# Kernel optimization log

Hardware: AMD Instinct MI355X
Metric: run time of the kernel (lower is better)

## Reference

```python
import jax, jax.numpy as jnp
import numpy as np

N_POINTS = 1_000_000
NUM_PILLARS = 30_000
BN_EPS = 1e-3


def _bn(x, gamma, beta, mean, var):
    # eval-mode BatchNorm1d with eps=0.001
    return (x - mean) * (gamma * jax.lax.rsqrt(var + BN_EPS)) + beta


def setup_inputs() -> dict:
    key = jax.random.key(0)
    ks = jax.random.split(key, 5)
    C1, C2 = 32, 64
    return {
        "points": jax.random.normal(ks[0], (N_POINTS, 5), dtype=jnp.float32),
        "f_center": jax.random.normal(ks[1], (N_POINTS, 3), dtype=jnp.float32),
        "unq_inv": jax.random.randint(ks[2], (N_POINTS,), 0, NUM_PILLARS, dtype=jnp.int32),
        "W1": jax.random.normal(ks[3], (7, C1), dtype=jnp.float32) * 0.1,
        "g1": jnp.ones((C1,), jnp.float32),
        "b1": jnp.zeros((C1,), jnp.float32),
        "m1": jnp.zeros((C1,), jnp.float32),
        "v1": jnp.ones((C1,), jnp.float32),
        "W2": jax.random.normal(ks[4], (C2, C1), dtype=jnp.float32) * 0.1,
        "g2": jnp.ones((C1,), jnp.float32),
        "b2": jnp.zeros((C1,), jnp.float32),
        "m2": jnp.zeros((C1,), jnp.float32),
        "v2": jnp.ones((C1,), jnp.float32),
    }


def reference(points, f_center, unq_inv, W1, g1, b1, m1, v1, W2, g2, b2, m2, v2):
    # gen_feat: concat(f_center, points[:,1:]) -> Linear(no bias) -> BN -> ReLU
    feats = jnp.concatenate([f_center, points[:, 1:]], axis=-1)  # [N, 7]
    h = jnp.maximum(_bn(feats @ W1, g1, b1, m1, v1), 0.0)        # [N, 32]

    # scatter_mean over pillars, then gather back and concat
    seg_sum = jax.ops.segment_sum(h, unq_inv, num_segments=NUM_PILLARS)
    counts = jax.ops.segment_sum(jnp.ones((h.shape[0],), h.dtype), unq_inv,
                                 num_segments=NUM_PILLARS)
    seg_mean = seg_sum / jnp.maximum(counts, 1.0)[:, None]       # [P, 32]
    h2 = jnp.concatenate([h, seg_mean[unq_inv]], axis=1)         # [N, 64]

    # AVFEO: Linear(64,32,no bias) -> BN -> ReLU
    out_fc = jnp.maximum(_bn(h2 @ W2, g2, b2, m2, v2), 0.0)      # [N, 32]

    # scatter_max over pillars (empty pillars -> 0, as torch_scatter)
    seg_max = jax.ops.segment_max(out_fc, unq_inv, num_segments=NUM_PILLARS)
    return jnp.where(jnp.isfinite(seg_max), seg_max, 0.0)        # [P, 32]
```

## Files before the change

### kernel.cpp

```cpp
#include <hip/hip_runtime.h>
#include <hip/hip_fp16.h>

typedef __attribute__((ext_vector_type(8))) short short8;
typedef __attribute__((ext_vector_type(4))) float floatx4;

static constexpr float EPS = 1e-3f;

#define PPB    16
#define NB     1875
#define CAPB   704
#define NBLK   64

#define P_W1F  0
#define P_B1F  224
#define P_W2L  256
#define P_B2F  1280
#define P_W2UT 1312
#define PREP_F 2048

__device__ __forceinline__ unsigned short f2bf(float x) {
  unsigned u = __float_as_uint(x);
  u += 0x7FFFu + ((u >> 16) & 1u);
  return (unsigned short)(u >> 16);
}
__device__ __forceinline__ unsigned pack2h(float a, float b) {
  __half2 h = __floats2half2_rn(a, b);
  return *reinterpret_cast<unsigned*>(&h);
}
__device__ __forceinline__ float2 unp2h(unsigned u) {
  __half2 h = *reinterpret_cast<__half2*>(&u);
  return __half22float2(h);
}
__device__ __forceinline__ unsigned fenc(float q) {
  unsigned u = __float_as_uint(q);
  return u ^ (0x80000000u | (unsigned)((int)u >> 31));
}

__global__ __launch_bounds__(1024)
void k_count(const int* __restrict__ unq, int* __restrict__ hist,
             const float* __restrict__ W1, const float* __restrict__ g1,
             const float* __restrict__ b1, const float* __restrict__ m1,
             const float* __restrict__ v1,
             const float* __restrict__ W2, const float* __restrict__ g2,
             const float* __restrict__ b2, const float* __restrict__ m2,
             const float* __restrict__ v2, float* __restrict__ prep, int N) {
  __shared__ int lh[NB];
  const int t = threadIdx.x, blk = blockIdx.x;
  for (int i = t; i < NB; i += 1024) lh[i] = 0;
  __syncthreads();
  const int chunk = (N + NBLK - 1) / NBLK;
  const int start = blk * chunk, end = min(start + chunk, N);
  for (int i = start + t; i < end; i += 1024) atomicAdd(&lh[unq[i] >> 4], 1);
  __syncthreads();
  for (int b = t; b < NB; b += 1024) hist[b * NBLK + blk] = lh[b];

  if (blk == 0) {
    for (int i = t; i < 224; i += 1024) {
      int c = i & 31;
      prep[P_W1F + i] = W1[i] * (g1[c] * rsqrtf(v1[c] + EPS));
    }
    if (t < 32) {
      float s1 = g1[t] * rsqrtf(v1[t] + EPS);
      float s2 = g2[t] * rsqrtf(v2[t] + EPS);
      prep[P_B1F + t] = b1[t] - m1[t] * s1;
      prep[P_B2F + t] = b2[t] - m2[t] * s2;
    }
    unsigned short* wt = (unsigned short*)(prep + P_W2UT);
    if (t < 1024) {
      int k = t >> 5, c = t & 31;
      float s2 = g2[c] * rsqrtf(v2[c] + EPS);
      prep[P_W2L + t] = W2[(32 + k) * 32 + c] * s2;
      wt[c * 32 + k] = f2bf(W2[k * 32 + c] * s2);
    }
  }
}

__global__ __launch_bounds__(256)
void k_scan(const int* __restrict__ hist, int* __restrict__ base,
            int* __restrict__ cntb) {
  const int w = threadIdx.x >> 6, lane = threadIdx.x & 63;
  const int b = blockIdx.x * 4 + w;
  if (b >= NB) return;
  int v = hist[b * NBLK + lane];
  int s = v;
#pragma unroll
  for (int d = 1; d < 64; d <<= 1) {
    int u = __shfl_up(s, d);
    if (lane >= d) s += u;
  }
  base[b * NBLK + lane] = b * CAPB + (s - v);
  if (lane == 63) cntb[b] = s;
}

__global__ __launch_bounds__(1024)
void k_scatter(const float* __restrict__ points, const float* __restrict__ fc,
               const int* __restrict__ unq, const int* __restrict__ base,
               uint4* __restrict__ barr, int N) {
  __shared__ int cur[NB];
  const int t = threadIdx.x, blk = blockIdx.x;
  for (int b = t; b < NB; b += 1024) cur[b] = base[b * NBLK + blk];
  __syncthreads();
  const int chunk = (N + NBLK - 1) / NBLK;
  const int start = blk * chunk, end = min(start + chunk, N);
  for (int i = start + t; i < end; i += 1024) {
    int p = unq[i];
    int b = p >> 4;
    float f0 = fc[3 * i], f1 = fc[3 * i + 1], f2v = fc[3 * i + 2];
    float f3 = points[5 * i + 1], f4 = points[5 * i + 2];
    float f5 = points[5 * i + 3], f6 = points[5 * i + 4];
    uint4 row;
    row.x = pack2h(f0, f1);
    row.y = pack2h(f2v, f3);
    row.z = pack2h(f4, f5);
    row.w = (pack2h(f6, 0.f) & 0xFFFFu) | ((unsigned)(p & 15) << 16);
    int pos = atomicAdd(&cur[b], 1);
    if (pos < (b + 1) * CAPB) barr[pos] = row;
  }
}

__global__ __launch_bounds__(256)
void k_bucket(const float* __restrict__ prep, const int* __restrict__ cntb,
              const uint4* __restrict__ barr, float* __restrict__ out) {
  __shared__ uint4 fbuf[CAPB];
  __shared__ __align__(16) unsigned short hbuf[CAPB * 32];
  __shared__ float psum[8][PPB * 32];
  __shared__ unsigned short pidb[CAPB];
  __shared__ int pcnt[PPB];
  __shared__ float pcl[PPB * 32];
  __shared__ unsigned omax[PPB * 33];
  __shared__ __align__(16) unsigned short w2t[1024];

  const int t = threadIdx.x, b = blockIdx.x;
  const int lane = t & 63, w = t >> 6;
  const int c = lane & 31, jg = t >> 5;

  int n = cntb[b];
  n = n < CAPB ? n : CAPB;

  for (int i = t; i < 8 * PPB * 32; i += 256) ((float*)psum)[i] = 0.f;
  for (int i = t; i < PPB * 33; i += 256) omax[i] = 0u;
  if (t < PPB) pcnt[t] = 0;
  ((uint2*)w2t)[t] = ((const uint2*)(prep + P_W2UT))[t];
  for (int i = t; i < n; i += 256) fbuf[i] = barr[(size_t)b * CAPB + i];
  __syncthreads();

  float w1c[7];
#pragma unroll
  for (int r = 0; r < 7; ++r) w1c[r] = prep[P_W1F + r * 32 + c];
  const float b1c = prep[P_B1F + c];
#pragma unroll 2
  for (int j = jg; j < n; j += 8) {
    uint4 rv = fbuf[j];
    float2 f01 = unp2h(rv.x), f23 = unp2h(rv.y), f45 = unp2h(rv.z);
    float f6 = unp2h(rv.w).x;
    int pid = rv.w >> 16;
    float d = f01.x * w1c[0];
    d = fmaf(f01.y, w1c[1], d);
    d = fmaf(f23.x, w1c[2], d);
    d = fmaf(f23.y, w1c[3], d);
    d = fmaf(f45.x, w1c[4], d);
    d = fmaf(f45.y, w1c[5], d);
    d = fmaf(f6,    w1c[6], d);
    float h = fmaxf(d + b1c, 0.f);
    hbuf[j * 32 + c] = f2bf(h);
    psum[jg][pid * 32 + c] += h;
    if (c == 0) pidb[j] = (unsigned short)pid;
  }
  __syncthreads();

  for (int j = t; j < n; j += 256) atomicAdd(&pcnt[pidb[j]], 1);
  for (int idx = t; idx < PPB * 32; idx += 256) {
    float s = psum[0][idx];
#pragma unroll
    for (int g = 1; g < 8; ++g) s += psum[g][idx];
    psum[0][idx] = s;
  }
  __syncthreads();

  for (int idx = t; idx < PPB * 32; idx += 256) {
    int pid = idx >> 5, cc = idx & 31;
    int np = pcnt[pid];
    float inv = np > 0 ? 1.f / (float)np : 0.f;
    float acc = 0.f;
    const floatx4* ms = (const floatx4*)&psum[0][pid * 32];
#pragma unroll
    for (int kq = 0; kq < 8; ++kq) {
      floatx4 sv = ms[kq];
      acc = fmaf(sv.x, prep[P_W2L + (kq * 4 + 0) * 32 + cc], acc);
      acc = fmaf(sv.y, prep[P_W2L + (kq * 4 + 1) * 32 + cc], acc);
      acc = fmaf(sv.z, prep[P_W2L + (kq * 4 + 2) * 32 + cc], acc);
      acc = fmaf(sv.w, prep[P_W2L + (kq * 4 + 3) * 32 + cc], acc);
    }
    pcl[idx] = fmaf(inv, acc, prep[P_B2F + cc]);
  }

  const int m16 = lane & 15, q4 = lane >> 4;
  short8 bf0 = *(const short8*)(w2t + m16 * 32 + q4 * 8);
  short8 bf1 = *(const short8*)(w2t + (m16 + 16) * 32 + q4 * 8);
  const int ntl = (n + 15) >> 4;
  for (int rt = w; rt < ntl; rt += 4) {
    short8 af = *(const short8*)(hbuf + (rt * 16 + m16) * 32 + q4 * 8);
    floatx4 z = {0.f, 0.f, 0.f, 0.f};
    floatx4 a0 = __builtin_amdgcn_mfma_f32_16x16x32_bf16(af, bf0, z, 0, 0, 0);
    floatx4 a1 = __builtin_amdgcn_mfma_f32_16x16x32_bf16(af, bf1, z, 0, 0, 0);
    const int rowb = rt * 16 + q4 * 4;
    uint2 pw = *(const uint2*)(pidb + rowb);
    int pid4[4] = {(int)(pw.x & 0xffffu), (int)(pw.x >> 16),
                   (int)(pw.y & 0xffffu), (int)(pw.y >> 16)};
#pragma unroll
    for (int r = 0; r < 4; ++r) {
      int row = rowb + r;
      if (row < n) {
        atomicMax(&omax[pid4[r] * 33 + m16],      fenc(a0[r]));
        atomicMax(&omax[pid4[r] * 33 + 16 + m16], fenc(a1[r]));
      }
    }
  }
  __syncthreads();

  for (int idx = t; idx < PPB * 32; idx += 256) {
    int pid = idx >> 5, cc = idx & 31;
    unsigned e = omax[pid * 33 + cc];
    float v = 0.f;
    if (e != 0u) {
      unsigned u = (e & 0x80000000u) ? (e ^ 0x80000000u) : ~e;
      v = fmaxf(__uint_as_float(u) + pcl[idx], 0.f);
    }
    out[(size_t)b * (PPB * 32) + idx] = v;
  }
}

extern "C" void kernel_launch(void* const* d_in, const int* in_sizes, int n_in,
                              void* d_out, int out_size, void* d_ws, size_t ws_size,
                              hipStream_t stream) {
  const float* points = (const float*)d_in[0];
  const float* fc     = (const float*)d_in[1];
  const int*   unq    = (const int*)d_in[2];
  const float* W1 = (const float*)d_in[3];
  const float* g1 = (const float*)d_in[4];
  const float* b1 = (const float*)d_in[5];
  const float* m1 = (const float*)d_in[6];
  const float* v1 = (const float*)d_in[7];
  const float* W2 = (const float*)d_in[8];
  const float* g2 = (const float*)d_in[9];
  const float* b2 = (const float*)d_in[10];
  const float* m2 = (const float*)d_in[11];
  const float* v2 = (const float*)d_in[12];

  const int N = in_sizes[0] / 5;

  int* hist = (int*)d_ws;
  int* base = hist + NB * NBLK;
  int* cntb = base + NB * NBLK;
  size_t off = (size_t)(2 * NB * NBLK + NB);
  off = (off + 255) & ~(size_t)255;
  float* prep = (float*)d_ws + off;
  size_t boff = off + PREP_F;
  boff = (boff + 255) & ~(size_t)255;
  uint4* barr = (uint4*)((float*)d_ws + boff);

  k_count<<<NBLK, 1024, 0, stream>>>(unq, hist, W1, g1, b1, m1, v1,
                                     W2, g2, b2, m2, v2, prep, N);
  k_scan<<<(NB + 3) / 4, 256, 0, stream>>>(hist, base, cntb);
  k_scatter<<<NBLK, 1024, 0, stream>>>(points, fc, unq, base, barr, N);
  k_bucket<<<NB, 256, 0, stream>>>(prep, cntb, barr, (float*)d_out);
}
```

Baseline: 197.7 us.

## Transpose histogram layout, add nontemporal loads, sort bucket rows by pillar

Histogram and base arrays now use a block-major layout, so the count and scatter kernels read and write them contiguously. The scan kernel stages a 64x64 tile in shared memory to transpose it before the prefix sum. Streaming input loads are marked nontemporal. In the bucket kernel, rows are counting-sorted by pillar in shared memory, and pillar sums are computed from the bf16 hidden buffer instead of eight replicated partial-sum arrays. This drops the per-group reduction but adds extra passes and barriers, and the mean now accumulates from bf16-rounded values.

```diff
diff --git a/kernel.cpp b/kernel.cpp
--- a/kernel.cpp
+++ b/kernel.cpp
@@ -22,6 +22,9 @@
   unsigned u = __float_as_uint(x);
   u += 0x7FFFu + ((u >> 16) & 1u);
   return (unsigned short)(u >> 16);
+}
+__device__ __forceinline__ float bf2f(unsigned short h) {
+  return __uint_as_float((unsigned)h << 16);
 }
 __device__ __forceinline__ unsigned pack2h(float a, float b) {
   __half2 h = __floats2half2_rn(a, b);
@@ -50,9 +53,10 @@
   __syncthreads();
   const int chunk = (N + NBLK - 1) / NBLK;
   const int start = blk * chunk, end = min(start + chunk, N);
-  for (int i = start + t; i < end; i += 1024) atomicAdd(&lh[unq[i] >> 4], 1);
-  __syncthreads();
-  for (int b = t; b < NB; b += 1024) hist[b * NBLK + blk] = lh[b];
+  for (int i = start + t; i < end; i += 1024)
+    atomicAdd(&lh[__builtin_nontemporal_load(&unq[i]) >> 4], 1);
+  __syncthreads();
+  for (int b = t; b < NB; b += 1024) hist[blk * NB + b] = lh[b];
 
   if (blk == 0) {
     for (int i = t; i < 224; i += 1024) {
@@ -78,18 +82,36 @@
 __global__ __launch_bounds__(256)
 void k_scan(const int* __restrict__ hist, int* __restrict__ base,
             int* __restrict__ cntb) {
-  const int w = threadIdx.x >> 6, lane = threadIdx.x & 63;
-  const int b = blockIdx.x * 4 + w;
-  if (b >= NB) return;
-  int v = hist[b * NBLK + lane];
-  int s = v;
-#pragma unroll
-  for (int d = 1; d < 64; d <<= 1) {
-    int u = __shfl_up(s, d);
-    if (lane >= d) s += u;
-  }
-  base[b * NBLK + lane] = b * CAPB + (s - v);
-  if (lane == 63) cntb[b] = s;
+  __shared__ int tile[64][65];
+  __shared__ int tot[64];
+  const int t = threadIdx.x, b0 = blockIdx.x * 64;
+  const int w = t >> 6, lane = t & 63;
+  for (int r0 = 0; r0 < 64; r0 += 4) {
+    int blk = r0 + (t >> 6), j = t & 63;
+    int v = 0;
+    if (b0 + j < NB) v = hist[blk * NB + b0 + j];
+    tile[j][blk] = v;
+  }
+  __syncthreads();
+  for (int k = 0; k < 16; ++k) {
+    int j = w * 16 + k;
+    int v = tile[j][lane];
+    int s = v;
+#pragma unroll
+    for (int d = 1; d < 64; d <<= 1) {
+      int u = __shfl_up(s, d);
+      if (lane >= d) s += u;
+    }
+    tile[j][lane] = s - v;
+    if (lane == 63) tot[j] = s;
+  }
+  __syncthreads();
+  for (int r0 = 0; r0 < 64; r0 += 4) {
+    int blk = r0 + (t >> 6), j = t & 63;
+    if (b0 + j < NB)
+      base[blk * NB + b0 + j] = (b0 + j) * CAPB + tile[j][blk];
+  }
+  if (t < 64 && b0 + t < NB) cntb[b0 + t] = tot[t];
 }
 
 __global__ __launch_bounds__(1024)
@@ -98,16 +120,20 @@
                uint4* __restrict__ barr, int N) {
   __shared__ int cur[NB];
   const int t = threadIdx.x, blk = blockIdx.x;
-  for (int b = t; b < NB; b += 1024) cur[b] = base[b * NBLK + blk];
+  for (int b = t; b < NB; b += 1024) cur[b] = base[blk * NB + b];
   __syncthreads();
   const int chunk = (N + NBLK - 1) / NBLK;
   const int start = blk * chunk, end = min(start + chunk, N);
   for (int i = start + t; i < end; i += 1024) {
-    int p = unq[i];
+    int p = __builtin_nontemporal_load(&unq[i]);
     int b = p >> 4;
-    float f0 = fc[3 * i], f1 = fc[3 * i + 1], f2v = fc[3 * i + 2];
-    float f3 = points[5 * i + 1], f4 = points[5 * i + 2];
-    float f5 = points[5 * i + 3], f6 = points[5 * i + 4];
+    float f0 = __builtin_nontemporal_load(&fc[3 * i]);
+    float f1 = __builtin_nontemporal_load(&fc[3 * i + 1]);
+    float f2v = __builtin_nontemporal_load(&fc[3 * i + 2]);
+    float f3 = __builtin_nontemporal_load(&points[5 * i + 1]);
+    float f4 = __builtin_nontemporal_load(&points[5 * i + 2]);
+    float f5 = __builtin_nontemporal_load(&points[5 * i + 3]);
+    float f6 = __builtin_nontemporal_load(&points[5 * i + 4]);
     uint4 row;
     row.x = pack2h(f0, f1);
     row.y = pack2h(f2v, f3);
@@ -123,12 +149,13 @@
               const uint4* __restrict__ barr, float* __restrict__ out) {
   __shared__ uint4 fbuf[CAPB];
   __shared__ __align__(16) unsigned short hbuf[CAPB * 32];
-  __shared__ float psum[8][PPB * 32];
+  __shared__ unsigned short sortpos[CAPB];
   __shared__ unsigned short pidb[CAPB];
-  __shared__ int pcnt[PPB];
+  __shared__ float psum[PPB * 32];
   __shared__ float pcl[PPB * 32];
   __shared__ unsigned omax[PPB * 33];
   __shared__ __align__(16) unsigned short w2t[1024];
+  __shared__ int pcnt[PPB], pilstart[PPB + 1], pilcur[PPB];
 
   const int t = threadIdx.x, b = blockIdx.x;
   const int lane = t & 63, w = t >> 6;
@@ -137,23 +164,47 @@
   int n = cntb[b];
   n = n < CAPB ? n : CAPB;
 
-  for (int i = t; i < 8 * PPB * 32; i += 256) ((float*)psum)[i] = 0.f;
   for (int i = t; i < PPB * 33; i += 256) omax[i] = 0u;
   if (t < PPB) pcnt[t] = 0;
   ((uint2*)w2t)[t] = ((const uint2*)(prep + P_W2UT))[t];
-  for (int i = t; i < n; i += 256) fbuf[i] = barr[(size_t)b * CAPB + i];
+  __syncthreads();
+  for (int i = t; i < n; i += 256) {
+    uint4 rv = barr[(size_t)b * CAPB + i];
+    fbuf[i] = rv;
+    atomicAdd(&pcnt[rv.w >> 16], 1);
+  }
+  __syncthreads();
+
+  if (t < 64) {
+    int v = (lane < PPB) ? pcnt[lane] : 0;
+    int s = v;
+#pragma unroll
+    for (int d = 1; d < PPB; d <<= 1) {
+      int u = __shfl_up(s, d);
+      if (lane >= d) s += u;
+    }
+    if (lane < PPB) { pilstart[lane] = s - v; pilcur[lane] = s - v; }
+    if (lane == PPB - 1) pilstart[PPB] = s;
+  }
+  __syncthreads();
+
+  for (int j = t; j < n; j += 256) {
+    int pid = fbuf[j].w >> 16;
+    int sp = atomicAdd(&pilcur[pid], 1);
+    sortpos[j] = (unsigned short)sp;
+    pidb[sp] = (unsigned short)pid;
+  }
   __syncthreads();
 
   float w1c[7];
 #pragma unroll
   for (int r = 0; r < 7; ++r) w1c[r] = prep[P_W1F + r * 32 + c];
   const float b1c = prep[P_B1F + c];
-#pragma unroll 2
   for (int j = jg; j < n; j += 8) {
     uint4 rv = fbuf[j];
+    int sp = sortpos[j];
     float2 f01 = unp2h(rv.x), f23 = unp2h(rv.y), f45 = unp2h(rv.z);
     float f6 = unp2h(rv.w).x;
-    int pid = rv.w >> 16;
     float d = f01.x * w1c[0];
     d = fmaf(f01.y, w1c[1], d);
     d = fmaf(f23.x, w1c[2], d);
@@ -162,27 +213,25 @@
     d = fmaf(f45.y, w1c[5], d);
     d = fmaf(f6,    w1c[6], d);
     float h = fmaxf(d + b1c, 0.f);
-    hbuf[j * 32 + c] = f2bf(h);
-    psum[jg][pid * 32 + c] += h;
-    if (c == 0) pidb[j] = (unsigned short)pid;
-  }
-  __syncthreads();
-
-  for (int j = t; j < n; j += 256) atomicAdd(&pcnt[pidb[j]], 1);
-  for (int idx = t; idx < PPB * 32; idx += 256) {
-    float s = psum[0][idx];
-#pragma unroll
-    for (int g = 1; g < 8; ++g) s += psum[g][idx];
-    psum[0][idx] = s;
+    hbuf[sp * 32 + c] = f2bf(h);
   }
   __syncthreads();
 
   for (int idx = t; idx < PPB * 32; idx += 256) {
     int pid = idx >> 5, cc = idx & 31;
-    int np = pcnt[pid];
+    int r0 = pilstart[pid], r1 = pilstart[pid + 1];
+    float s = 0.f;
+    for (int r = r0; r < r1; ++r) s += bf2f(hbuf[r * 32 + cc]);
+    psum[idx] = s;
+  }
+  __syncthreads();
+
+  for (int idx = t; idx < PPB * 32; idx += 256) {
+    int pid = idx >> 5, cc = idx & 31;
+    int np = pilstart[pid + 1] - pilstart[pid];
     float inv = np > 0 ? 1.f / (float)np : 0.f;
     float acc = 0.f;
-    const floatx4* ms = (const floatx4*)&psum[0][pid * 32];
+    const floatx4* ms = (const floatx4*)&psum[pid * 32];
 #pragma unroll
     for (int kq = 0; kq < 8; ++kq) {
       floatx4 sv = ms[kq];
@@ -250,9 +299,9 @@
   const int N = in_sizes[0] / 5;
 
   int* hist = (int*)d_ws;
-  int* base = hist + NB * NBLK;
-  int* cntb = base + NB * NBLK;
-  size_t off = (size_t)(2 * NB * NBLK + NB);
+  int* base = hist + NBLK * NB;
+  int* cntb = base + NBLK * NB;
+  size_t off = (size_t)(2 * NBLK * NB + NB);
   off = (off + 255) & ~(size_t)255;
   float* prep = (float*)d_ws + off;
   size_t boff = off + PREP_F;
@@ -261,7 +310,7 @@
 
   k_count<<<NBLK, 1024, 0, stream>>>(unq, hist, W1, g1, b1, m1, v1,
                                      W2, g2, b2, m2, v2, prep, N);
-  k_scan<<<(NB + 3) / 4, 256, 0, stream>>>(hist, base, cntb);
+  k_scan<<<(NB + 63) / 64, 256, 0, stream>>>(hist, base, cntb);
   k_scatter<<<NBLK, 1024, 0, stream>>>(points, fc, unq, base, barr, N);
   k_bucket<<<NB, 256, 0, stream>>>(prep, cntb, barr, (float*)d_out);
 }
```

New measurement: 223.3 us. 12.9% more time.
